# Performance work log

Hardware: AMD Instinct MI355X
Metric: run time of the kernel (lower is better)

Reference implementation:

```python
import jax, jax.numpy as jnp
import numpy as np

N_EMBD = 1024
N_HEAD = 16
HEAD_DIM = N_EMBD // N_HEAD


def setup_inputs() -> dict:
    key = jax.random.key(0)
    ks = jax.random.split(key, 9)
    B, T, C = 4, 2048, N_EMBD
    s = 1.0 / np.sqrt(C)
    return {
        "x": jax.random.normal(ks[0], (B, T, C), dtype=jnp.float32),
        "Wk": jax.random.normal(ks[1], (C, C), dtype=jnp.float32) * s,
        "bk": jax.random.normal(ks[2], (C,), dtype=jnp.float32) * 0.02,
        "Wq": jax.random.normal(ks[3], (C, C), dtype=jnp.float32) * s,
        "bq": jax.random.normal(ks[4], (C,), dtype=jnp.float32) * 0.02,
        "Wv": jax.random.normal(ks[5], (C, C), dtype=jnp.float32) * s,
        "bv": jax.random.normal(ks[6], (C,), dtype=jnp.float32) * 0.02,
        "Wp": jax.random.normal(ks[7], (C, C), dtype=jnp.float32) * s,
        "bp": jax.random.normal(ks[8], (C,), dtype=jnp.float32) * 0.02,
    }


def reference(x, Wk, bk, Wq, bq, Wv, bv, Wp, bp):
    B, T, C = x.shape
    nh, hs = N_HEAD, HEAD_DIM
    # linear projections; weights stored as [in, out] (x @ W + b)
    k = (x @ Wk + bk).reshape(B, T, nh, hs).transpose(0, 2, 1, 3)  # [B,nh,T,hs]
    q = (x @ Wq + bq).reshape(B, T, nh, hs).transpose(0, 2, 1, 3)
    v = (x @ Wv + bv).reshape(B, T, nh, hs).transpose(0, 2, 1, 3)
    att = jnp.einsum("bhqd,bhkd->bhqk", q, k) / jnp.sqrt(jnp.float32(hs))
    causal = jnp.tril(jnp.ones((T, T), dtype=bool))  # [T,T]
    att = jnp.where(causal[None, None], att, -jnp.inf)
    att = jax.nn.softmax(att, axis=-1)
    y = jnp.einsum("bhqk,bhkd->bhqd", att, v)  # [B,nh,T,hs]
    y = y.transpose(0, 2, 1, 3).reshape(B, T, C)
    return y @ Wp + bp
```

## Files before the change

kernel.cpp:

```cpp
#include <hip/hip_runtime.h>

#define TSEQ 2048
#define CDIM 1024
#define NH 16
#define HS 64
#define BATCH 4

typedef __attribute__((ext_vector_type(8))) short short8;
typedef __attribute__((ext_vector_type(4))) short s16x4;
typedef __attribute__((ext_vector_type(4))) float f32x4;

__device__ __forceinline__ short f2bf(float f) {
    unsigned u = __builtin_bit_cast(unsigned, f);
    unsigned r = (u + 0x7fffu + ((u >> 16) & 1u)) >> 16;
    return (short)r;
}

__device__ __forceinline__ void gload_lds16(const void* g, void* l) {
    __builtin_amdgcn_global_load_lds((const __attribute__((address_space(1))) void*)g,
                                     (__attribute__((address_space(3))) void*)l, 16, 0, 0);
}

__global__ void cvt_x(const float* __restrict__ x, short* __restrict__ o, int n4) {
    int i = blockIdx.x * 256 + threadIdx.x;
    if (i >= n4) return;
    float4 v = ((const float4*)x)[i];
    s16x4 r;
    r[0] = f2bf(v.x); r[1] = f2bf(v.y); r[2] = f2bf(v.z); r[3] = f2bf(v.w);
    ((s16x4*)o)[i] = r;
}

__global__ void wtrans(const float* __restrict__ Wk, const float* __restrict__ Wq,
                       const float* __restrict__ Wv, const float* __restrict__ Wp,
                       short* __restrict__ Wcat, short* __restrict__ Wpt) {
    const float* src; short* dst;
    if (blockIdx.z == 0)      { src = Wq; dst = Wcat; }
    else if (blockIdx.z == 1) { src = Wk; dst = Wcat + 1048576; }
    else if (blockIdx.z == 2) { src = Wv; dst = Wcat + 2097152; }
    else                      { src = Wp; dst = Wpt; }
    __shared__ float tl[64][65];
    int tx = threadIdx.x & 63, ty = threadIdx.x >> 6;
    int k0 = blockIdx.x * 64, n0 = blockIdx.y * 64;
#pragma unroll
    for (int i = 0; i < 16; ++i) {
        int r = i * 4 + ty;
        tl[r][tx] = src[(size_t)(k0 + r) * CDIM + n0 + tx];
    }
    __syncthreads();
#pragma unroll
    for (int i = 0; i < 16; ++i) {
        int r = i * 4 + ty;
        dst[(size_t)(n0 + r) * CDIM + k0 + tx] = f2bf(tl[tx][r]);
    }
}

__global__ void bias_pack(const float* __restrict__ bq, const float* __restrict__ bk,
                          const float* __restrict__ bv, float* __restrict__ bcat) {
    int i = blockIdx.x * 256 + threadIdx.x;
    if (i < 1024) bcat[i] = bq[i];
    else if (i < 2048) bcat[i] = bk[i - 1024];
    else if (i < 3072) bcat[i] = bv[i - 2048];
}

template <bool OUT_BF16, bool VSPLIT>
__global__ __launch_bounds__(256) void gemm_bt(const short* __restrict__ A, int lda,
                                               const short* __restrict__ Bt,
                                               const float* __restrict__ bias,
                                               float alphaQ, int qcols,
                                               void* __restrict__ Cout, int ldc,
                                               short* __restrict__ Vt) {
    __shared__ short As[128 * 64];
    __shared__ short Bs[128 * 64];
    const int t = threadIdx.x;
    const int lane = t & 63, w = t >> 6;
    const int lr = lane & 15, lg = lane >> 4;
    const int wr = w >> 1, wc = w & 1;
    const int mbase = blockIdx.y * 128, nbase = blockIdx.x * 128;
    const float alpha = (nbase < qcols) ? alphaQ : 1.0f;
    f32x4 acc[4][4] = {};
    for (int k0 = 0; k0 < 1024; k0 += 64) {
#pragma unroll
        for (int i = 0; i < 4; ++i) {
            int chunk = i * 256 + t;
            int r = chunk >> 3, c = chunk & 7;
            int cl = c ^ (r & 7);
            gload_lds16(A + (size_t)(mbase + r) * lda + k0 + cl * 8, As + chunk * 8);
            gload_lds16(Bt + (size_t)(nbase + r) * 1024 + k0 + cl * 8, Bs + chunk * 8);
        }
        __syncthreads();
#pragma unroll
        for (int ks = 0; ks < 2; ++ks) {
            short8 a[4], b[4];
#pragma unroll
            for (int mi = 0; mi < 4; ++mi) {
                int row = wr * 64 + mi * 16 + lr;
                int ch = (ks * 4 + lg) ^ (row & 7);
                a[mi] = *(const short8*)(As + row * 64 + ch * 8);
            }
#pragma unroll
            for (int ni = 0; ni < 4; ++ni) {
                int row = wc * 64 + ni * 16 + lr;
                int ch = (ks * 4 + lg) ^ (row & 7);
                b[ni] = *(const short8*)(Bs + row * 64 + ch * 8);
            }
#pragma unroll
            for (int mi = 0; mi < 4; ++mi)
#pragma unroll
                for (int ni = 0; ni < 4; ++ni)
                    acc[mi][ni] = __builtin_amdgcn_mfma_f32_16x16x32_bf16(a[mi], b[ni],
                                                                          acc[mi][ni], 0, 0, 0);
        }
        __syncthreads();
    }
    if (VSPLIT && nbase >= 2048) {
        const int btok = mbase & (TSEQ - 1);
        const int bidx = mbase >> 11;
#pragma unroll
        for (int mi = 0; mi < 4; ++mi) {
#pragma unroll
            for (int ni = 0; ni < 4; ++ni) {
                const int col = nbase + wc * 64 + ni * 16 + lr;
                const int dfull = col - 2048;
                const float bv = bias[col];
                const int tok0 = btok + wr * 64 + mi * 16 + lg * 4;
                s16x4 pk;
#pragma unroll
                for (int ii = 0; ii < 4; ++ii) pk[ii] = f2bf(acc[mi][ni][ii] + bv);
                *(s16x4*)(Vt + (size_t)(bidx * 1024 + dfull) * TSEQ + tok0) = pk;
            }
        }
        return;
    }
#pragma unroll
    for (int mi = 0; mi < 4; ++mi) {
#pragma unroll
        for (int ni = 0; ni < 4; ++ni) {
            int col = nbase + wc * 64 + ni * 16 + lr;
            float bv = bias[col];
#pragma unroll
            for (int i = 0; i < 4; ++i) {
                int row = mbase + wr * 64 + mi * 16 + lg * 4 + i;
                float v = (acc[mi][ni][i] + bv) * alpha;
                if (OUT_BF16)
                    ((short*)Cout)[(size_t)row * ldc + col] = f2bf(v);
                else
                    ((float*)Cout)[(size_t)row * ldc + col] = v;
            }
        }
    }
}

__global__ __launch_bounds__(512, 4) void attn(const short* __restrict__ QKV,
                                               const short* __restrict__ Vt,
                                               short* __restrict__ Y) {
    __shared__ short Kl[2][64 * 64];
    __shared__ short Vl[2][64 * 64];
    __shared__ short Pl[8][16 * 64];
    const int t = threadIdx.x, lane = t & 63, w = t >> 6;
    const int lr = lane & 15, lg = lane >> 4;
    const int bh = blockIdx.x, b = bh >> 4, h = bh & 15;
    const int qt = 15 - blockIdx.y;
    const int q0w = qt * 128 + w * 16;
    const size_t rowbase = (size_t)b * TSEQ;
    const int niter = 2 * qt + 2;
    const float SHIFT2 = 17.31234049f;

    short8 qf[2];
#pragma unroll
    for (int ks = 0; ks < 2; ++ks)
        qf[ks] = *(const short8*)(QKV + (rowbase + q0w + lr) * 3072 + h * HS + ks * 32 + lg * 8);
    float l_i[4] = {0.f, 0.f, 0.f, 0.f};
    f32x4 o[4] = {};

    const int sr = t >> 3, sc = t & 7, scl = sc ^ (sr & 7);
    const short* Kg = QKV + 1024 + h * HS;
    gload_lds16(Kg + (rowbase + sr) * 3072 + scl * 8, &Kl[0][t * 8]);
    gload_lds16(Vt + (size_t)(bh * 64 + sr) * TSEQ + scl * 8, &Vl[0][t * 8]);
    __syncthreads();
    int buf = 0;
    for (int jt = 0; jt < niter; ++jt) {
        const int j0 = jt * 64;
        if (jt + 1 < niter) {
            const int j0n = j0 + 64;
            gload_lds16(Kg + (rowbase + j0n + sr) * 3072 + scl * 8, &Kl[buf ^ 1][t * 8]);
            gload_lds16(Vt + (size_t)(bh * 64 + sr) * TSEQ + j0n + scl * 8, &Vl[buf ^ 1][t * 8]);
        }
        if (j0 <= q0w + 15) {
            f32x4 s[4];
            __builtin_amdgcn_s_setprio(1);
#pragma unroll
            for (int nt = 0; nt < 4; ++nt) {
                s[nt] = f32x4{0.f, 0.f, 0.f, 0.f};
#pragma unroll
                for (int ks = 0; ks < 2; ++ks) {
                    short8 kf = *(const short8*)(&Kl[buf][(nt * 16 + lr) * 64 +
                                                          (((ks * 4 + lg) ^ (lr & 7)) * 8)]);
                    s[nt] = __builtin_amdgcn_mfma_f32_16x16x32_bf16(qf[ks], kf, s[nt], 0, 0, 0);
                }
            }
            __builtin_amdgcn_s_setprio(0);
            if (j0 + 63 > q0w) {
#pragma unroll
                for (int nt = 0; nt < 4; ++nt)
#pragma unroll
                    for (int i = 0; i < 4; ++i) {
                        int kv = j0 + nt * 16 + lr;
                        int q = q0w + lg * 4 + i;
                        if (kv > q) s[nt][i] = -__builtin_inff();
                    }
            }
#pragma unroll
            for (int i = 0; i < 4; ++i) {
                const int ql = lg * 4 + i;
                float pt[4];
#pragma unroll
                for (int nt = 0; nt < 4; ++nt) {
                    float p = __builtin_amdgcn_exp2f(s[nt][i] - SHIFT2);
                    unsigned u = __builtin_bit_cast(unsigned, p);
                    int chv = ((nt * 2 + (lr >> 3)) ^ (ql & 7));
                    Pl[w][ql * 64 + chv * 8 + (lr & 7)] = (short)(u >> 16);
                    pt[nt] = __builtin_bit_cast(float, u & 0xffff0000u);
                }
                l_i[i] += (pt[0] + pt[1]) + (pt[2] + pt[3]);
            }
            short8 pf[2];
#pragma unroll
            for (int ks = 0; ks < 2; ++ks)
                pf[ks] = *(const short8*)(&Pl[w][lr * 64 + (((ks * 4 + lg) ^ (lr & 7)) * 8)]);
            __builtin_amdgcn_s_setprio(1);
#pragma unroll
            for (int nd = 0; nd < 4; ++nd)
#pragma unroll
                for (int ks = 0; ks < 2; ++ks) {
                    short8 vf = *(const short8*)(&Vl[buf][(nd * 16 + lr) * 64 +
                                                          (((ks * 4 + lg) ^ (lr & 7)) * 8)]);
                    o[nd] = __builtin_amdgcn_mfma_f32_16x16x32_bf16(pf[ks], vf, o[nd], 0, 0, 0);
                }
            __builtin_amdgcn_s_setprio(0);
        }
        __syncthreads();
        buf ^= 1;
    }
#pragma unroll
    for (int i = 0; i < 4; ++i) {
        float l = l_i[i];
        l += __shfl_xor(l, 1);
        l += __shfl_xor(l, 2);
        l += __shfl_xor(l, 4);
        l += __shfl_xor(l, 8);
        float inv = 1.0f / l;
        int q = q0w + lg * 4 + i;
#pragma unroll
        for (int nd = 0; nd < 4; ++nd)
            Y[(rowbase + q) * 1024 + h * HS + nd * 16 + lr] = f2bf(o[nd][i] * inv);
    }
}

extern "C" void kernel_launch(void* const* d_in, const int* in_sizes, int n_in,
                              void* d_out, int out_size, void* d_ws, size_t ws_size,
                              hipStream_t stream) {
    const float* x  = (const float*)d_in[0];
    const float* Wk = (const float*)d_in[1];
    const float* bk = (const float*)d_in[2];
    const float* Wq = (const float*)d_in[3];
    const float* bq = (const float*)d_in[4];
    const float* Wv = (const float*)d_in[5];
    const float* bv = (const float*)d_in[6];
    const float* Wp = (const float*)d_in[7];
    const float* bp = (const float*)d_in[8];
    float* out = (float*)d_out;
    char* ws = (char*)d_ws;
    const size_t MB = 1024 * 1024;
    short* xb   = (short*)(ws);
    short* Wcat = (short*)(ws + 16 * MB);
    short* Wpt  = (short*)(ws + 22 * MB);
    short* QKVb = (short*)(ws + 24 * MB);
    short* Yb   = xb;
    short* VtT  = (short*)d_out;
    float* bcat = (float*)((char*)d_out + 16 * MB);

    const float alphaQ = 0.125f * 1.44269504088896f;

    cvt_x<<<8192, 256, 0, stream>>>(x, xb, 2097152);
    wtrans<<<dim3(16, 16, 4), 256, 0, stream>>>(Wk, Wq, Wv, Wp, Wcat, Wpt);
    bias_pack<<<12, 256, 0, stream>>>(bq, bk, bv, bcat);
    gemm_bt<true, true><<<dim3(24, 64), 256, 0, stream>>>(xb, 1024, Wcat, bcat, alphaQ, 1024,
                                                          QKVb, 3072, VtT);
    attn<<<dim3(64, 16), 512, 0, stream>>>(QKVb, VtT, Yb);
    gemm_bt<false, false><<<dim3(8, 64), 256, 0, stream>>>(Yb, 1024, Wpt, bp, 1.0f, 0,
                                                           out, 1024, nullptr);
}
```

Before: 170.1 us.

## Retile QKV GEMM to 256x96 and pair causal attention tiles per block

```diff
diff --git a/kernel.cpp b/kernel.cpp
--- a/kernel.cpp
+++ b/kernel.cpp
@@ -62,13 +62,96 @@
     else if (i < 3072) bcat[i] = bv[i - 2048];
 }
 
-template <bool OUT_BF16, bool VSPLIT>
-__global__ __launch_bounds__(256) void gemm_bt(const short* __restrict__ A, int lda,
+__global__ __launch_bounds__(512, 4) void gemm96(const short* __restrict__ A,
+                                                 const short* __restrict__ Bt,
+                                                 const float* __restrict__ bias,
+                                                 float alphaQ,
+                                                 short* __restrict__ C,
+                                                 short* __restrict__ Vt) {
+    __shared__ short As[256 * 64];
+    __shared__ short Bs[96 * 64];
+    const int t = threadIdx.x;
+    const int lane = t & 63, w = t >> 6;
+    const int lr = lane & 15, lg = lane >> 4;
+    const int wr = w >> 1, wc = w & 1;
+    const int tl = (blockIdx.x & 7) * 128 + (blockIdx.x >> 3);
+    const int mbase = (tl >> 5) * 256, nbase = (tl & 31) * 96;
+    f32x4 acc[4][3] = {};
+    for (int k0 = 0; k0 < 1024; k0 += 64) {
+#pragma unroll
+        for (int i = 0; i < 4; ++i) {
+            int chunk = i * 512 + t;
+            int r = chunk >> 3, c = chunk & 7;
+            int cl = c ^ (r & 7);
+            gload_lds16(A + (size_t)(mbase + r) * 1024 + k0 + cl * 8, As + chunk * 8);
+        }
+        {
+            int r = t >> 3, c = t & 7;
+            int cl = c ^ (r & 7);
+            gload_lds16(Bt + (size_t)(nbase + r) * 1024 + k0 + cl * 8, Bs + t * 8);
+            if (t < 256) {
+                int chunk = 512 + t;
+                int r2 = chunk >> 3, c2 = chunk & 7;
+                int cl2 = c2 ^ (r2 & 7);
+                gload_lds16(Bt + (size_t)(nbase + r2) * 1024 + k0 + cl2 * 8, Bs + chunk * 8);
+            }
+        }
+        __syncthreads();
+#pragma unroll
+        for (int ks = 0; ks < 2; ++ks) {
+            short8 a[4], b[3];
+#pragma unroll
+            for (int mi = 0; mi < 4; ++mi) {
+                int row = wr * 64 + mi * 16 + lr;
+                int ch = (ks * 4 + lg) ^ (row & 7);
+                a[mi] = *(const short8*)(As + row * 64 + ch * 8);
+            }
+#pragma unroll
+            for (int ni = 0; ni < 3; ++ni) {
+                int row = wc * 48 + ni * 16 + lr;
+                int ch = (ks * 4 + lg) ^ (row & 7);
+                b[ni] = *(const short8*)(Bs + row * 64 + ch * 8);
+            }
+#pragma unroll
+            for (int mi = 0; mi < 4; ++mi)
+#pragma unroll
+                for (int ni = 0; ni < 3; ++ni)
+                    acc[mi][ni] = __builtin_amdgcn_mfma_f32_16x16x32_bf16(a[mi], b[ni],
+                                                                          acc[mi][ni], 0, 0, 0);
+        }
+        __syncthreads();
+    }
+    const int btok = mbase & (TSEQ - 1);
+    const int bidx = mbase >> 11;
+#pragma unroll
+    for (int mi = 0; mi < 4; ++mi) {
+#pragma unroll
+        for (int ni = 0; ni < 3; ++ni) {
+            const int col = nbase + wc * 48 + ni * 16 + lr;
+            const float bv = bias[col];
+            if (col >= 2048) {
+                const int dfull = col - 2048;
+                const int tok0 = btok + wr * 64 + mi * 16 + lg * 4;
+                s16x4 pk;
+#pragma unroll
+                for (int ii = 0; ii < 4; ++ii) pk[ii] = f2bf(acc[mi][ni][ii] + bv);
+                *(s16x4*)(Vt + (size_t)(bidx * 1024 + dfull) * TSEQ + tok0) = pk;
+            } else {
+                const float alpha = (col < 1024) ? alphaQ : 1.0f;
+#pragma unroll
+                for (int ii = 0; ii < 4; ++ii) {
+                    const int row = mbase + wr * 64 + mi * 16 + lg * 4 + ii;
+                    C[(size_t)row * 3072 + col] = f2bf((acc[mi][ni][ii] + bv) * alpha);
+                }
+            }
+        }
+    }
+}
+
+__global__ __launch_bounds__(256) void gemm_bt(const short* __restrict__ A,
                                                const short* __restrict__ Bt,
                                                const float* __restrict__ bias,
-                                               float alphaQ, int qcols,
-                                               void* __restrict__ Cout, int ldc,
-                                               short* __restrict__ Vt) {
+                                               float* __restrict__ Cout) {
     __shared__ short As[128 * 64];
     __shared__ short Bs[128 * 64];
     const int t = threadIdx.x;
@@ -76,7 +159,6 @@
     const int lr = lane & 15, lg = lane >> 4;
     const int wr = w >> 1, wc = w & 1;
     const int mbase = blockIdx.y * 128, nbase = blockIdx.x * 128;
-    const float alpha = (nbase < qcols) ? alphaQ : 1.0f;
     f32x4 acc[4][4] = {};
     for (int k0 = 0; k0 < 1024; k0 += 64) {
 #pragma unroll
@@ -84,7 +166,7 @@
             int chunk = i * 256 + t;
             int r = chunk >> 3, c = chunk & 7;
             int cl = c ^ (r & 7);
-            gload_lds16(A + (size_t)(mbase + r) * lda + k0 + cl * 8, As + chunk * 8);
+            gload_lds16(A + (size_t)(mbase + r) * 1024 + k0 + cl * 8, As + chunk * 8);
             gload_lds16(Bt + (size_t)(nbase + r) * 1024 + k0 + cl * 8, Bs + chunk * 8);
         }
         __syncthreads();
@@ -112,25 +194,6 @@
         }
         __syncthreads();
     }
-    if (VSPLIT && nbase >= 2048) {
-        const int btok = mbase & (TSEQ - 1);
-        const int bidx = mbase >> 11;
-#pragma unroll
-        for (int mi = 0; mi < 4; ++mi) {
-#pragma unroll
-            for (int ni = 0; ni < 4; ++ni) {
-                const int col = nbase + wc * 64 + ni * 16 + lr;
-                const int dfull = col - 2048;
-                const float bv = bias[col];
-                const int tok0 = btok + wr * 64 + mi * 16 + lg * 4;
-                s16x4 pk;
-#pragma unroll
-                for (int ii = 0; ii < 4; ++ii) pk[ii] = f2bf(acc[mi][ni][ii] + bv);
-                *(s16x4*)(Vt + (size_t)(bidx * 1024 + dfull) * TSEQ + tok0) = pk;
-            }
-        }
-        return;
-    }
 #pragma unroll
     for (int mi = 0; mi < 4; ++mi) {
 #pragma unroll
@@ -140,52 +203,59 @@
 #pragma unroll
             for (int i = 0; i < 4; ++i) {
                 int row = mbase + wr * 64 + mi * 16 + lg * 4 + i;
-                float v = (acc[mi][ni][i] + bv) * alpha;
-                if (OUT_BF16)
-                    ((short*)Cout)[(size_t)row * ldc + col] = f2bf(v);
-                else
-                    ((float*)Cout)[(size_t)row * ldc + col] = v;
-            }
-        }
-    }
-}
-
-__global__ __launch_bounds__(512, 4) void attn(const short* __restrict__ QKV,
+                Cout[(size_t)row * 1024 + col] = acc[mi][ni][i] + bv;
+            }
+        }
+    }
+}
+
+__global__ __launch_bounds__(256, 4) void attn(const short* __restrict__ QKV,
                                                const short* __restrict__ Vt,
                                                short* __restrict__ Y) {
     __shared__ short Kl[2][64 * 64];
     __shared__ short Vl[2][64 * 64];
-    __shared__ short Pl[8][16 * 64];
+    __shared__ short Pl[4][16 * 64];
     const int t = threadIdx.x, lane = t & 63, w = t >> 6;
     const int lr = lane & 15, lg = lane >> 4;
-    const int bh = blockIdx.x, b = bh >> 4, h = bh & 15;
-    const int qt = 15 - blockIdx.y;
-    const int q0w = qt * 128 + w * 16;
+    const int bid = blockIdx.x;
+    const int cx = bid & 7, sx = bid >> 3;
+    const int bh = cx * 8 + (sx >> 4), pb = sx & 15;
+    const int b = bh >> 4, h = bh & 15;
     const size_t rowbase = (size_t)b * TSEQ;
-    const int niter = 2 * qt + 2;
     const float SHIFT2 = 17.31234049f;
-
-    short8 qf[2];
-#pragma unroll
-    for (int ks = 0; ks < 2; ++ks)
-        qf[ks] = *(const short8*)(QKV + (rowbase + q0w + lr) * 3072 + h * HS + ks * 32 + lg * 8);
-    float l_i[4] = {0.f, 0.f, 0.f, 0.f};
-    f32x4 o[4] = {};
-
     const int sr = t >> 3, sc = t & 7, scl = sc ^ (sr & 7);
     const short* Kg = QKV + 1024 + h * HS;
-    gload_lds16(Kg + (rowbase + sr) * 3072 + scl * 8, &Kl[0][t * 8]);
-    gload_lds16(Vt + (size_t)(bh * 64 + sr) * TSEQ + scl * 8, &Vl[0][t * 8]);
-    __syncthreads();
-    int buf = 0;
-    for (int jt = 0; jt < niter; ++jt) {
-        const int j0 = jt * 64;
-        if (jt + 1 < niter) {
-            const int j0n = j0 + 64;
-            gload_lds16(Kg + (rowbase + j0n + sr) * 3072 + scl * 8, &Kl[buf ^ 1][t * 8]);
-            gload_lds16(Vt + (size_t)(bh * 64 + sr) * TSEQ + j0n + scl * 8, &Vl[buf ^ 1][t * 8]);
-        }
-        if (j0 <= q0w + 15) {
+
+    const int useg0 = 31 - pb, useg1 = pb;
+    for (int sg = 0; sg < 2; ++sg) {
+        const int u = sg ? useg1 : useg0;
+        const int q0w = u * 64 + w * 16;
+        const int niter = u + 1;
+        short8 qf[2];
+#pragma unroll
+        for (int ks = 0; ks < 2; ++ks)
+            qf[ks] = *(const short8*)(QKV + (rowbase + q0w + lr) * 3072 + h * HS +
+                                      ks * 32 + lg * 8);
+        float l_i[4] = {0.f, 0.f, 0.f, 0.f};
+        f32x4 o[4] = {};
+        gload_lds16(Kg + (rowbase + sr) * 3072 + scl * 8, &Kl[0][t * 8]);
+        gload_lds16(Kg + (rowbase + 32 + sr) * 3072 + scl * 8, &Kl[0][(256 + t) * 8]);
+        gload_lds16(Vt + (size_t)(bh * 64 + sr) * TSEQ + scl * 8, &Vl[0][t * 8]);
+        gload_lds16(Vt + (size_t)(bh * 64 + 32 + sr) * TSEQ + scl * 8, &Vl[0][(256 + t) * 8]);
+        __syncthreads();
+        int buf = 0;
+        for (int jt = 0; jt < niter; ++jt) {
+            const int j0 = jt * 64;
+            if (jt + 1 < niter) {
+                const int j0n = j0 + 64;
+                gload_lds16(Kg + (rowbase + j0n + sr) * 3072 + scl * 8, &Kl[buf ^ 1][t * 8]);
+                gload_lds16(Kg + (rowbase + j0n + 32 + sr) * 3072 + scl * 8,
+                            &Kl[buf ^ 1][(256 + t) * 8]);
+                gload_lds16(Vt + (size_t)(bh * 64 + sr) * TSEQ + j0n + scl * 8,
+                            &Vl[buf ^ 1][t * 8]);
+                gload_lds16(Vt + (size_t)(bh * 64 + 32 + sr) * TSEQ + j0n + scl * 8,
+                            &Vl[buf ^ 1][(256 + t) * 8]);
+            }
             f32x4 s[4];
             __builtin_amdgcn_s_setprio(1);
 #pragma unroll
@@ -199,7 +269,7 @@
                 }
             }
             __builtin_amdgcn_s_setprio(0);
-            if (j0 + 63 > q0w) {
+            if (jt == niter - 1) {
 #pragma unroll
                 for (int nt = 0; nt < 4; ++nt)
 #pragma unroll
@@ -216,10 +286,10 @@
 #pragma unroll
                 for (int nt = 0; nt < 4; ++nt) {
                     float p = __builtin_amdgcn_exp2f(s[nt][i] - SHIFT2);
-                    unsigned u = __builtin_bit_cast(unsigned, p);
+                    unsigned uu = __builtin_bit_cast(unsigned, p);
                     int chv = ((nt * 2 + (lr >> 3)) ^ (ql & 7));
-                    Pl[w][ql * 64 + chv * 8 + (lr & 7)] = (short)(u >> 16);
-                    pt[nt] = __builtin_bit_cast(float, u & 0xffff0000u);
+                    Pl[w][ql * 64 + chv * 8 + (lr & 7)] = (short)(uu >> 16);
+                    pt[nt] = __builtin_bit_cast(float, uu & 0xffff0000u);
                 }
                 l_i[i] += (pt[0] + pt[1]) + (pt[2] + pt[3]);
             }
@@ -237,22 +307,23 @@
                     o[nd] = __builtin_amdgcn_mfma_f32_16x16x32_bf16(pf[ks], vf, o[nd], 0, 0, 0);
                 }
             __builtin_amdgcn_s_setprio(0);
-        }
-        __syncthreads();
-        buf ^= 1;
-    }
-#pragma unroll
-    for (int i = 0; i < 4; ++i) {
-        float l = l_i[i];
-        l += __shfl_xor(l, 1);
-        l += __shfl_xor(l, 2);
-        l += __shfl_xor(l, 4);
-        l += __shfl_xor(l, 8);
-        float inv = 1.0f / l;
-        int q = q0w + lg * 4 + i;
-#pragma unroll
-        for (int nd = 0; nd < 4; ++nd)
-            Y[(rowbase + q) * 1024 + h * HS + nd * 16 + lr] = f2bf(o[nd][i] * inv);
+            __syncthreads();
+            buf ^= 1;
+        }
+#pragma unroll
+        for (int i = 0; i < 4; ++i) {
+            float l = l_i[i];
+            l += __shfl_xor(l, 1);
+            l += __shfl_xor(l, 2);
+            l += __shfl_xor(l, 4);
+            l += __shfl_xor(l, 8);
+            float inv = 1.0f / l;
+            int q = q0w + lg * 4 + i;
+#pragma unroll
+            for (int nd = 0; nd < 4; ++nd)
+                Y[(rowbase + q) * 1024 + h * HS + nd * 16 + lr] = f2bf(o[nd][i] * inv);
+        }
+        __syncthreads();
     }
 }
 
@@ -284,9 +355,7 @@
     cvt_x<<<8192, 256, 0, stream>>>(x, xb, 2097152);
     wtrans<<<dim3(16, 16, 4), 256, 0, stream>>>(Wk, Wq, Wv, Wp, Wcat, Wpt);
     bias_pack<<<12, 256, 0, stream>>>(bq, bk, bv, bcat);
-    gemm_bt<true, true><<<dim3(24, 64), 256, 0, stream>>>(xb, 1024, Wcat, bcat, alphaQ, 1024,
-                                                          QKVb, 3072, VtT);
-    attn<<<dim3(64, 16), 512, 0, stream>>>(QKVb, VtT, Yb);
-    gemm_bt<false, false><<<dim3(8, 64), 256, 0, stream>>>(Yb, 1024, Wpt, bp, 1.0f, 0,
-                                                           out, 1024, nullptr);
-}
+    gemm96<<<1024, 512, 0, stream>>>(xb, Wcat, bcat, alphaQ, QKVb, VtT);
+    attn<<<1024, 256, 0, stream>>>(QKVb, VtT, Yb);
+    gemm_bt<<<dim3(8, 64), 256, 0, stream>>>(Yb, Wpt, bp, out);
+}
```

Result: faster. 165.6 us (-2.6%).

## Pair causal query tiles per block for balanced attention work and remap grid

Applied to the files above, without the earlier changes.

```diff
diff --git a/kernel.cpp b/kernel.cpp
--- a/kernel.cpp
+++ b/kernel.cpp
@@ -150,42 +150,53 @@
     }
 }
 
-__global__ __launch_bounds__(512, 4) void attn(const short* __restrict__ QKV,
+__global__ __launch_bounds__(256, 4) void attn(const short* __restrict__ QKV,
                                                const short* __restrict__ Vt,
                                                short* __restrict__ Y) {
     __shared__ short Kl[2][64 * 64];
     __shared__ short Vl[2][64 * 64];
-    __shared__ short Pl[8][16 * 64];
+    __shared__ short Pl[4][16 * 64];
     const int t = threadIdx.x, lane = t & 63, w = t >> 6;
     const int lr = lane & 15, lg = lane >> 4;
-    const int bh = blockIdx.x, b = bh >> 4, h = bh & 15;
-    const int qt = 15 - blockIdx.y;
-    const int q0w = qt * 128 + w * 16;
+    const int bid = blockIdx.x;
+    const int cx = bid & 7, sx = bid >> 3;
+    const int bh = cx * 8 + (sx >> 4), pb = sx & 15;
+    const int b = bh >> 4, h = bh & 15;
     const size_t rowbase = (size_t)b * TSEQ;
-    const int niter = 2 * qt + 2;
     const float SHIFT2 = 17.31234049f;
-
-    short8 qf[2];
-#pragma unroll
-    for (int ks = 0; ks < 2; ++ks)
-        qf[ks] = *(const short8*)(QKV + (rowbase + q0w + lr) * 3072 + h * HS + ks * 32 + lg * 8);
-    float l_i[4] = {0.f, 0.f, 0.f, 0.f};
-    f32x4 o[4] = {};
-
     const int sr = t >> 3, sc = t & 7, scl = sc ^ (sr & 7);
     const short* Kg = QKV + 1024 + h * HS;
-    gload_lds16(Kg + (rowbase + sr) * 3072 + scl * 8, &Kl[0][t * 8]);
-    gload_lds16(Vt + (size_t)(bh * 64 + sr) * TSEQ + scl * 8, &Vl[0][t * 8]);
-    __syncthreads();
-    int buf = 0;
-    for (int jt = 0; jt < niter; ++jt) {
-        const int j0 = jt * 64;
-        if (jt + 1 < niter) {
-            const int j0n = j0 + 64;
-            gload_lds16(Kg + (rowbase + j0n + sr) * 3072 + scl * 8, &Kl[buf ^ 1][t * 8]);
-            gload_lds16(Vt + (size_t)(bh * 64 + sr) * TSEQ + j0n + scl * 8, &Vl[buf ^ 1][t * 8]);
-        }
-        if (j0 <= q0w + 15) {
+
+    const int useg0 = 31 - pb, useg1 = pb;
+    for (int sg = 0; sg < 2; ++sg) {
+        const int u = sg ? useg1 : useg0;
+        const int q0w = u * 64 + w * 16;
+        const int niter = u + 1;
+        short8 qf[2];
+#pragma unroll
+        for (int ks = 0; ks < 2; ++ks)
+            qf[ks] = *(const short8*)(QKV + (rowbase + q0w + lr) * 3072 + h * HS +
+                                      ks * 32 + lg * 8);
+        float l_i[4] = {0.f, 0.f, 0.f, 0.f};
+        f32x4 o[4] = {};
+        gload_lds16(Kg + (rowbase + sr) * 3072 + scl * 8, &Kl[0][t * 8]);
+        gload_lds16(Kg + (rowbase + 32 + sr) * 3072 + scl * 8, &Kl[0][(256 + t) * 8]);
+        gload_lds16(Vt + (size_t)(bh * 64 + sr) * TSEQ + scl * 8, &Vl[0][t * 8]);
+        gload_lds16(Vt + (size_t)(bh * 64 + 32 + sr) * TSEQ + scl * 8, &Vl[0][(256 + t) * 8]);
+        __syncthreads();
+        int buf = 0;
+        for (int jt = 0; jt < niter; ++jt) {
+            const int j0 = jt * 64;
+            if (jt + 1 < niter) {
+                const int j0n = j0 + 64;
+                gload_lds16(Kg + (rowbase + j0n + sr) * 3072 + scl * 8, &Kl[buf ^ 1][t * 8]);
+                gload_lds16(Kg + (rowbase + j0n + 32 + sr) * 3072 + scl * 8,
+                            &Kl[buf ^ 1][(256 + t) * 8]);
+                gload_lds16(Vt + (size_t)(bh * 64 + sr) * TSEQ + j0n + scl * 8,
+                            &Vl[buf ^ 1][t * 8]);
+                gload_lds16(Vt + (size_t)(bh * 64 + 32 + sr) * TSEQ + j0n + scl * 8,
+                            &Vl[buf ^ 1][(256 + t) * 8]);
+            }
             f32x4 s[4];
             __builtin_amdgcn_s_setprio(1);
 #pragma unroll
@@ -199,7 +210,7 @@
                 }
             }
             __builtin_amdgcn_s_setprio(0);
-            if (j0 + 63 > q0w) {
+            if (jt == niter - 1) {
 #pragma unroll
                 for (int nt = 0; nt < 4; ++nt)
 #pragma unroll
@@ -216,10 +227,10 @@
 #pragma unroll
                 for (int nt = 0; nt < 4; ++nt) {
                     float p = __builtin_amdgcn_exp2f(s[nt][i] - SHIFT2);
-                    unsigned u = __builtin_bit_cast(unsigned, p);
+                    unsigned uu = __builtin_bit_cast(unsigned, p);
                     int chv = ((nt * 2 + (lr >> 3)) ^ (ql & 7));
-                    Pl[w][ql * 64 + chv * 8 + (lr & 7)] = (short)(u >> 16);
-                    pt[nt] = __builtin_bit_cast(float, u & 0xffff0000u);
+                    Pl[w][ql * 64 + chv * 8 + (lr & 7)] = (short)(uu >> 16);
+                    pt[nt] = __builtin_bit_cast(float, uu & 0xffff0000u);
                 }
                 l_i[i] += (pt[0] + pt[1]) + (pt[2] + pt[3]);
             }
@@ -237,22 +248,23 @@
                     o[nd] = __builtin_amdgcn_mfma_f32_16x16x32_bf16(pf[ks], vf, o[nd], 0, 0, 0);
                 }
             __builtin_amdgcn_s_setprio(0);
+            __syncthreads();
+            buf ^= 1;
+        }
+#pragma unroll
+        for (int i = 0; i < 4; ++i) {
+            float l = l_i[i];
+            l += __shfl_xor(l, 1);
+            l += __shfl_xor(l, 2);
+            l += __shfl_xor(l, 4);
+            l += __shfl_xor(l, 8);
+            float inv = 1.0f / l;
+            int q = q0w + lg * 4 + i;
+#pragma unroll
+            for (int nd = 0; nd < 4; ++nd)
+                Y[(rowbase + q) * 1024 + h * HS + nd * 16 + lr] = f2bf(o[nd][i] * inv);
         }
         __syncthreads();
-        buf ^= 1;
-    }
-#pragma unroll
-    for (int i = 0; i < 4; ++i) {
-        float l = l_i[i];
-        l += __shfl_xor(l, 1);
-        l += __shfl_xor(l, 2);
-        l += __shfl_xor(l, 4);
-        l += __shfl_xor(l, 8);
-        float inv = 1.0f / l;
-        int q = q0w + lg * 4 + i;
-#pragma unroll
-        for (int nd = 0; nd < 4; ++nd)
-            Y[(rowbase + q) * 1024 + h * HS + nd * 16 + lr] = f2bf(o[nd][i] * inv);
     }
 }
 
@@ -284,9 +296,9 @@
     cvt_x<<<8192, 256, 0, stream>>>(x, xb, 2097152);
     wtrans<<<dim3(16, 16, 4), 256, 0, stream>>>(Wk, Wq, Wv, Wp, Wcat, Wpt);
     bias_pack<<<12, 256, 0, stream>>>(bq, bk, bv, bcat);
-    gemm_bt<true, true><<<dim3(24, 64), 256, 0, stream>>>(xb, 1024, Wcat, bcat, alphaQ, 1024,
-                                                          QKVb, 3072, VtT);
-    attn<<<dim3(64, 16), 512, 0, stream>>>(QKVb, VtT, Yb);
+    gemm_bt<true, true><<<dim3(24, 64), 256, 16384, stream>>>(xb, 1024, Wcat, bcat, alphaQ,
+                                                              1024, QKVb, 3072, VtT);
+    attn<<<1024, 256, 0, stream>>>(QKVb, VtT, Yb);
     gemm_bt<false, false><<<dim3(8, 64), 256, 0, stream>>>(Yb, 1024, Wpt, bp, 1.0f, 0,
                                                            out, 1024, nullptr);
 }
```

Result: slower. 174.6 us (+2.7%).
